# Optimization experiments

Hardware: AMD Instinct MI355X
Metric: run time of the kernel (lower is better)

The kernel has to match this reference:

```python
import jax, jax.numpy as jnp
import numpy as np

H = 10  # LSTM hidden size (hardcoded in the torch module)


def setup_inputs() -> dict:
    key = jax.random.key(0)
    ks = jax.random.split(key, 7)
    B, T, I = 16384, 512, 6
    s = 1.0 / np.sqrt(H)  # torch default init scale
    x = jax.random.normal(ks[0], (B, T, I), dtype=jnp.float32)
    W_ih = jax.random.uniform(ks[1], (4 * H, I), jnp.float32, -s, s)
    W_hh = jax.random.uniform(ks[2], (4 * H, H), jnp.float32, -s, s)
    b_ih = jax.random.uniform(ks[3], (4 * H,), jnp.float32, -s, s)
    b_hh = jax.random.uniform(ks[4], (4 * H,), jnp.float32, -s, s)
    W_fc = jax.random.uniform(ks[5], (2, H), jnp.float32, -s, s)
    b_fc = jax.random.uniform(ks[6], (2,), jnp.float32, -s, s)
    return {"x": x, "W_ih": W_ih, "W_hh": W_hh, "b_ih": b_ih,
            "b_hh": b_hh, "W_fc": W_fc, "b_fc": b_fc}


def reference(x, W_ih, W_hh, b_ih, b_hh, W_fc, b_fc):
    B = x.shape[0]
    # Precompute input-to-gate projections for all timesteps: [B, T, 4H]
    xg = jnp.einsum("bti,gi->btg", x, W_ih) + b_ih + b_hh

    def step(carry, xt):
        h, c = carry
        gates = xt + h @ W_hh.T                       # [B, 4H]
        i, f, g, o = jnp.split(gates, 4, axis=-1)     # torch gate order i,f,g,o
        i = jax.nn.sigmoid(i)
        f = jax.nn.sigmoid(f)
        g = jnp.tanh(g)
        o = jax.nn.sigmoid(o)
        c = f * c + i * g
        h = o * jnp.tanh(c)
        return (h, c), None

    h0 = jnp.zeros((B, H), x.dtype)
    (h_last, _), _ = jax.lax.scan(step, (h0, h0), jnp.swapaxes(xg, 0, 1))
    # Final-timestep hidden state -> FC -> sigmoid
    return jax.nn.sigmoid(h_last @ W_fc.T + b_fc)
```

## Files before the change

kernel.cpp:

```cpp
#include <hip/hip_runtime.h>

typedef float f32x4  __attribute__((ext_vector_type(4)));
typedef short bf16x8 __attribute__((ext_vector_type(8)));

#define SEQT 512
#define TC   16
#define NCH  (SEQT/TC)
#define ROWDW 68
#define BUFDW (16*ROWDW)

#define FEXP2(v) __builtin_amdgcn_exp2f(v)
#define FRCP(v)  __builtin_amdgcn_rcpf(v)
__device__ __forceinline__ unsigned pkbf(float a, float b){ unsigned r; asm("v_cvt_pk_bf16_f32 %0, %1, %2":"=v"(r):"v"(a),"v"(b)); return r; }
__device__ __forceinline__ float sigm (float s){ return FRCP(1.0f + FEXP2(s * -1.4426950408889634f)); }

union FragU { unsigned u[4]; bf16x8 v; uint4 q; };

__device__ __forceinline__ int unit_of(int cg, int t){
    if (t==0) return cg==0 ? 0 : cg==1 ? 4 : cg==2 ? 2 : 9;
    if (t==1) return cg==0 ? 1 : cg==1 ? 5 : cg==2 ? 3 : 8;
    return      cg==0 ? -1 : cg==1 ? 6 : cg==2 ? -1 : 7;
}
__device__ __forceinline__ int zslot(int k){
    if (k < 6)  return k;
    if (k == 6) return 6;
    if (k == 7) return 7;
    if (k == 8) return 10;
    if (k == 9) return 11;
    if (k == 10) return 12;
    if (k == 11) return 13;
    if (k == 16) return 8;
    if (k == 17) return 9;
    if (k == 24) return 15;
    if (k == 25) return 14;
    return -1;
}

__device__ __forceinline__ void cell(const f32x4 a, float& c, float& h){
    const float K1 = -1.4426950408889634f;
    const float K2 = -2.8853900817779268f;
    float Ei = FEXP2(a[0]*K1);
    float Ef = FEXP2(a[1]*K1);
    float Eg = FEXP2(a[2]*K2);
    float Eo = FEXP2(a[3]*K1);
    float P  = (1.0f+Ei)*(1.0f+Eg);
    float Q  = 1.0f+Ef;
    float r  = FRCP(P*Q);
    float ig = (1.0f-Eg)*Q*r;
    float sf = P*r;
    c = fmaf(sf, c, ig);
    float Ec  = FEXP2(c*K2);
    float roc = FRCP((1.0f+Eo)*(1.0f+Ec));
    h = (1.0f-Ec)*roc;
}

__global__ __launch_bounds__(256)
__attribute__((amdgpu_waves_per_eu(1, 1)))
void Model_88459146428723_kernel(const float* __restrict__ x,
                                 const float* __restrict__ Wih,
                                 const float* __restrict__ Whh,
                                 const float* __restrict__ bih,
                                 const float* __restrict__ bhh,
                                 const float* __restrict__ Wfc,
                                 const float* __restrict__ bfc,
                                 float* __restrict__ out)
{
    __shared__ unsigned xbf[4][2*BUFDW];
    __shared__ float hfin[4][16][12];

    const int tid = threadIdx.x;
    const int wv = tid >> 6, l = tid & 63, m = l & 15, gq = l >> 4;

    FragU wf[3];
    #pragma unroll
    for (int t=0; t<3; ++t){
        const int u  = unit_of(m>>2, t);
        const int gt = m & 3;
        float av[8];
        #pragma unroll
        for (int j=0; j<8; ++j){
            const int z = zslot(8*gq + j);
            float v = 0.0f;
            if (u >= 0 && z >= 0){
                const int row = gt*10 + u;
                v = (z < 6) ? Wih[row*6 + z] : Whh[row*10 + (z-6)];
            }
            av[j] = v;
        }
        #pragma unroll
        for (int w=0; w<4; ++w) wf[t].u[w] = pkbf(av[2*w], av[2*w+1]);
    }
    f32x4 bias[3];
    #pragma unroll
    for (int t=0; t<3; ++t){
        const int u = unit_of(gq, t);
        #pragma unroll
        for (int jD=0; jD<4; ++jD)
            bias[t][jD] = (u>=0) ? (bih[jD*10+u] + bhh[jD*10+u]) : 0.0f;
    }

    const float* xwb = x + (size_t)(blockIdx.x*64 + wv*16) * (SEQT*6);
    unsigned* myx = &xbf[wv][0];
    float4 stg[6];

    auto load_ch = [&](int ch){
        #pragma unroll
        for (int k=0; k<6; ++k){
            const int f = l + 64*k, mb = f/24, c4 = f%24;
            stg[k] = *reinterpret_cast<const float4*>(xwb + (size_t)mb*(SEQT*6) + ch*(TC*6) + c4*4);
        }
    };
    auto write_buf = [&](int buf){
        unsigned* dst = myx + buf*BUFDW;
        #pragma unroll
        for (int k=0; k<6; ++k){
            const int f = l + 64*k, mb = f/24, c4 = f%24;
            const int P0 = 2*c4, P1 = P0+1;
            dst[mb*ROWDW + (P0/3)*4 + (P0%3)] = pkbf(stg[k].x, stg[k].y);
            dst[mb*ROWDW + (P1/3)*4 + (P1%3)] = pkbf(stg[k].z, stg[k].w);
        }
    };

    load_ch(0); write_buf(0);
    uint4 xw = *reinterpret_cast<const uint4*>(myx + m*ROWDW);

    const bool is_g0 = (gq==0), is_g1 = (gq==1);

    unsigned B0 = is_g0 ? xw.x : 0u;
    unsigned B1 = is_g0 ? xw.y : 0u;
    unsigned B2 = is_g0 ? xw.z : 0u;
    unsigned B3 = 0u;
    float c0=0.f, c1=0.f, c2=0.f;
    float ht0=0.f, ht1=0.f, ht2=0.f;

    #pragma unroll 1
    for (int ch=0; ch<NCH; ++ch){
        const int cur = ch & 1;
        if (ch+1 < NCH) load_ch(ch+1);
        const unsigned* abase = myx + cur*BUFDW + m*ROWDW;
        const unsigned* bbase = myx + (cur^1)*BUFDW + m*ROWDW;

        #pragma unroll
        for (int tt=0; tt<TC; ++tt){
            FragU Bf; Bf.u[0]=B0; Bf.u[1]=B1; Bf.u[2]=B2; Bf.u[3]=B3;
            f32x4 a0 = __builtin_amdgcn_mfma_f32_16x16x32_bf16(wf[0].v, Bf.v, bias[0], 0,0,0);
            f32x4 a1 = __builtin_amdgcn_mfma_f32_16x16x32_bf16(wf[1].v, Bf.v, bias[1], 0,0,0);
            f32x4 a2 = __builtin_amdgcn_mfma_f32_16x16x32_bf16(wf[2].v, Bf.v, bias[2], 0,0,0);

            uint4 xwn;
            if (tt < 15) xwn = *reinterpret_cast<const uint4*>(abase + (tt+1)*4);
            else         xwn = *reinterpret_cast<const uint4*>(bbase);

            cell(a0, c0, ht0);
            cell(a1, c1, ht1);
            cell(a2, c2, ht2);

            if (tt==14 && ch+1<NCH) write_buf(cur^1);

            const unsigned pkA = pkbf(ht0, ht1);
            unsigned sa = __float_as_uint(ht2), sb = sa;
            asm("v_permlane32_swap_b32 %0, %1" : "+v"(sa), "+v"(sb));
            const unsigned pkB = pkbf(ht2, __uint_as_float(sb));

            B0 = is_g0 ? xwn.x : pkA;
            B1 = is_g0 ? xwn.y : (is_g1 ? pkB : 0u);
            B2 = is_g0 ? xwn.z : 0u;
            B3 = is_g0 ? pkA   : 0u;
        }
    }

    {
        const int ua = unit_of(gq,0);            hfin[wv][m][ua] = ht0;
        const int ub = unit_of(gq,1);            hfin[wv][m][ub] = ht1;
        const int uc = unit_of(gq,2); if (uc>=0) hfin[wv][m][uc] = ht2;
    }
    __syncthreads();
    if (l < 32){
        const int j = l >> 4, mm = l & 15;
        float a = bfc[j];
        #pragma unroll
        for (int u=0; u<10; ++u) a = fmaf(Wfc[j*10+u], hfin[wv][mm][u], a);
        out[(size_t)(blockIdx.x*64 + wv*16 + mm)*2 + j] = sigm(a);
    }
}

extern "C" void kernel_launch(void* const* d_in, const int* in_sizes, int n_in,
                              void* d_out, int out_size, void* d_ws, size_t ws_size,
                              hipStream_t stream) {
    const float* x   = (const float*)d_in[0];
    const float* Wih = (const float*)d_in[1];
    const float* Whh = (const float*)d_in[2];
    const float* bih = (const float*)d_in[3];
    const float* bhh = (const float*)d_in[4];
    const float* Wfc = (const float*)d_in[5];
    const float* bfc = (const float*)d_in[6];
    float* out = (float*)d_out;

    dim3 grid(16384 / 64);
    dim3 block(256);
    Model_88459146428723_kernel<<<grid, block, 0, stream>>>(x, Wih, Whh, bih, bhh, Wfc, bfc, out);
}
```

Before: 153.8 us.

## Split each wave's batch tile into two interleaved half-tile recurrence streams

Each wave now runs two independent LSTM recurrence streams, A and B. Stream A handles batch rows 0-7 and stream B handles rows 8-15, with each row duplicated across the 16 MFMA columns. Each timestep issues six MFMAs and six cell evaluations instead of three, interleaved, so one stream's latency can hide behind the other's arithmetic. The cost is twice the MFMA and transcendental work per step for the same 16 batch rows. The permlane swap also moves into a helper with explicit register moves.

```diff
diff --git a/kernel.cpp b/kernel.cpp
--- a/kernel.cpp
+++ b/kernel.cpp
@@ -13,6 +13,16 @@
 #define FRCP(v)  __builtin_amdgcn_rcpf(v)
 __device__ __forceinline__ unsigned pkbf(float a, float b){ unsigned r; asm("v_cvt_pk_bf16_f32 %0, %1, %2":"=v"(r):"v"(a),"v"(b)); return r; }
 __device__ __forceinline__ float sigm (float s){ return FRCP(1.0f + FEXP2(s * -1.4426950408889634f)); }
+
+__device__ __forceinline__ unsigned swap_hi32(float v){
+    unsigned dst, src;
+    asm("v_mov_b32 %0, %2\n\t"
+        "v_mov_b32 %1, %2\n\t"
+        "v_permlane32_swap_b32 %0, %1"
+        : "=&v"(dst), "=&v"(src)
+        : "v"(__float_as_uint(v)));
+    return src;
+}
 
 union FragU { unsigned u[4]; bf16x8 v; uint4 q; };
 
@@ -122,57 +132,80 @@
     };
 
     load_ch(0); write_buf(0);
-    uint4 xw = *reinterpret_cast<const uint4*>(myx + m*ROWDW);
+
+    const int mA = m & 7;
+    const int mB = 8 + (m & 7);
+    uint4 xwA = *reinterpret_cast<const uint4*>(myx + mA*ROWDW);
+    uint4 xwB = *reinterpret_cast<const uint4*>(myx + mB*ROWDW);
 
     const bool is_g0 = (gq==0), is_g1 = (gq==1);
 
-    unsigned B0 = is_g0 ? xw.x : 0u;
-    unsigned B1 = is_g0 ? xw.y : 0u;
-    unsigned B2 = is_g0 ? xw.z : 0u;
-    unsigned B3 = 0u;
-    float c0=0.f, c1=0.f, c2=0.f;
-    float ht0=0.f, ht1=0.f, ht2=0.f;
+    unsigned A0  = is_g0 ? xwA.x : 0u, A1  = is_g0 ? xwA.y : 0u, A2  = is_g0 ? xwA.z : 0u, A3  = 0u;
+    unsigned Bb0 = is_g0 ? xwB.x : 0u, Bb1 = is_g0 ? xwB.y : 0u, Bb2 = is_g0 ? xwB.z : 0u, Bb3 = 0u;
+    float cA0=0.f, cA1=0.f, cA2=0.f, hA0=0.f, hA1=0.f, hA2=0.f;
+    float cB0=0.f, cB1=0.f, cB2=0.f, hB0=0.f, hB1=0.f, hB2=0.f;
 
     #pragma unroll 1
     for (int ch=0; ch<NCH; ++ch){
         const int cur = ch & 1;
         if (ch+1 < NCH) load_ch(ch+1);
-        const unsigned* abase = myx + cur*BUFDW + m*ROWDW;
-        const unsigned* bbase = myx + (cur^1)*BUFDW + m*ROWDW;
+        const unsigned* aA = myx + cur*BUFDW + mA*ROWDW;
+        const unsigned* aB = myx + cur*BUFDW + mB*ROWDW;
+        const unsigned* bA = myx + (cur^1)*BUFDW + mA*ROWDW;
+        const unsigned* bB = myx + (cur^1)*BUFDW + mB*ROWDW;
 
         #pragma unroll
         for (int tt=0; tt<TC; ++tt){
-            FragU Bf; Bf.u[0]=B0; Bf.u[1]=B1; Bf.u[2]=B2; Bf.u[3]=B3;
-            f32x4 a0 = __builtin_amdgcn_mfma_f32_16x16x32_bf16(wf[0].v, Bf.v, bias[0], 0,0,0);
-            f32x4 a1 = __builtin_amdgcn_mfma_f32_16x16x32_bf16(wf[1].v, Bf.v, bias[1], 0,0,0);
-            f32x4 a2 = __builtin_amdgcn_mfma_f32_16x16x32_bf16(wf[2].v, Bf.v, bias[2], 0,0,0);
-
-            uint4 xwn;
-            if (tt < 15) xwn = *reinterpret_cast<const uint4*>(abase + (tt+1)*4);
-            else         xwn = *reinterpret_cast<const uint4*>(bbase);
-
-            cell(a0, c0, ht0);
-            cell(a1, c1, ht1);
-            cell(a2, c2, ht2);
+            FragU FA; FA.u[0]=A0;  FA.u[1]=A1;  FA.u[2]=A2;  FA.u[3]=A3;
+            FragU FB; FB.u[0]=Bb0; FB.u[1]=Bb1; FB.u[2]=Bb2; FB.u[3]=Bb3;
+            f32x4 a0A = __builtin_amdgcn_mfma_f32_16x16x32_bf16(wf[0].v, FA.v, bias[0], 0,0,0);
+            f32x4 a1A = __builtin_amdgcn_mfma_f32_16x16x32_bf16(wf[1].v, FA.v, bias[1], 0,0,0);
+            f32x4 a2A = __builtin_amdgcn_mfma_f32_16x16x32_bf16(wf[2].v, FA.v, bias[2], 0,0,0);
+            f32x4 a0B = __builtin_amdgcn_mfma_f32_16x16x32_bf16(wf[0].v, FB.v, bias[0], 0,0,0);
+            f32x4 a1B = __builtin_amdgcn_mfma_f32_16x16x32_bf16(wf[1].v, FB.v, bias[1], 0,0,0);
+            f32x4 a2B = __builtin_amdgcn_mfma_f32_16x16x32_bf16(wf[2].v, FB.v, bias[2], 0,0,0);
+
+            uint4 xwnA, xwnB;
+            if (tt < 15){ xwnA = *reinterpret_cast<const uint4*>(aA + (tt+1)*4);
+                          xwnB = *reinterpret_cast<const uint4*>(aB + (tt+1)*4); }
+            else        { xwnA = *reinterpret_cast<const uint4*>(bA);
+                          xwnB = *reinterpret_cast<const uint4*>(bB); }
+
+            cell(a0A, cA0, hA0);
+            cell(a0B, cB0, hB0);
+            cell(a1A, cA1, hA1);
+            cell(a1B, cB1, hB1);
+            cell(a2A, cA2, hA2);
+            cell(a2B, cB2, hB2);
 
             if (tt==14 && ch+1<NCH) write_buf(cur^1);
 
-            const unsigned pkA = pkbf(ht0, ht1);
-            unsigned sa = __float_as_uint(ht2), sb = sa;
-            asm("v_permlane32_swap_b32 %0, %1" : "+v"(sa), "+v"(sb));
-            const unsigned pkB = pkbf(ht2, __uint_as_float(sb));
-
-            B0 = is_g0 ? xwn.x : pkA;
-            B1 = is_g0 ? xwn.y : (is_g1 ? pkB : 0u);
-            B2 = is_g0 ? xwn.z : 0u;
-            B3 = is_g0 ? pkA   : 0u;
-        }
-    }
-
-    {
-        const int ua = unit_of(gq,0);            hfin[wv][m][ua] = ht0;
-        const int ub = unit_of(gq,1);            hfin[wv][m][ub] = ht1;
-        const int uc = unit_of(gq,2); if (uc>=0) hfin[wv][m][uc] = ht2;
+            {
+                const unsigned pA = pkbf(hA0, hA1);
+                const unsigned pB = pkbf(hA2, __uint_as_float(swap_hi32(hA2)));
+                A0 = is_g0 ? xwnA.x : pA;
+                A1 = is_g0 ? xwnA.y : (is_g1 ? pB : 0u);
+                A2 = is_g0 ? xwnA.z : 0u;
+                A3 = is_g0 ? pA     : 0u;
+            }
+            {
+                const unsigned pA = pkbf(hB0, hB1);
+                const unsigned pB = pkbf(hB2, __uint_as_float(swap_hi32(hB2)));
+                Bb0 = is_g0 ? xwnB.x : pA;
+                Bb1 = is_g0 ? xwnB.y : (is_g1 ? pB : 0u);
+                Bb2 = is_g0 ? xwnB.z : 0u;
+                Bb3 = is_g0 ? pA     : 0u;
+            }
+        }
+    }
+
+    if (m < 8){
+        const int ua = unit_of(gq,0);
+        const int ub = unit_of(gq,1);
+        const int uc = unit_of(gq,2);
+        hfin[wv][m][ua]   = hA0;  hfin[wv][m+8][ua]   = hB0;
+        hfin[wv][m][ub]   = hA1;  hfin[wv][m+8][ub]   = hB1;
+        if (uc>=0){ hfin[wv][m][uc] = hA2; hfin[wv][m+8][uc] = hB2; }
     }
     __syncthreads();
     if (l < 32){
```

Result: slower. 259.9 us (+69.0%).
